# Performance work log

Hardware: AMD Instinct MI355X
Metric: run time of the kernel (lower is better)

## Reference

```python
import jax, jax.numpy as jnp
import numpy as np

N_NODES = 100000

def _scatter_mean(vals, idx, num_segments):
    # vals: [E, D], idx: [E] -> [num_segments, D], mean with zero-degree -> 0 (PyG clamps count to 1)
    s = jax.ops.segment_sum(vals, idx, num_segments=num_segments)
    cnt = jax.ops.segment_sum(jnp.ones((vals.shape[0],), vals.dtype), idx, num_segments=num_segments)
    return s / jnp.maximum(cnt, 1.0)[:, None]

def _conv(x, edge_index, W1, W2, Wr, br):
    src, dst = edge_index[0], edge_index[1]
    n = x.shape[0]
    # flow source_to_target: aggregate lin1(x)[src] at dst
    out1 = _scatter_mean((x @ W1)[src], dst, n)
    # flow target_to_source: aggregate lin2(x)[dst] at src
    out2 = _scatter_mean((x @ W2)[dst], src, n)
    return x @ Wr + br + out1 + out2

def setup_inputs() -> dict:
    key = jax.random.key(0)
    ks = jax.random.split(key, 10)
    d_in, d_h, E = 64, 64, 1250000
    x = jax.random.normal(ks[0], (N_NODES, d_in), dtype=jnp.float32)
    edge_index = jax.random.randint(ks[1], (2, E), 0, N_NODES)
    def lin(k, fan_in, fan_out):
        bound = 1.0 / np.sqrt(fan_in)
        return jax.random.uniform(k, (fan_in, fan_out), jnp.float32, -bound, bound)
    inp = {"x": x, "edge_index": edge_index}
    inp["W1_0"] = lin(ks[2], d_in, d_h)
    inp["W2_0"] = lin(ks[3], d_in, d_h)
    inp["Wr_0"] = lin(ks[4], d_in, d_h)
    inp["br_0"] = jax.random.uniform(ks[5], (d_h,), jnp.float32, -1/np.sqrt(d_in), 1/np.sqrt(d_in))
    inp["W1_1"] = lin(ks[6], d_h, d_h)
    inp["W2_1"] = lin(ks[7], d_h, d_h)
    inp["Wr_1"] = lin(ks[8], d_h, d_h)
    inp["br_1"] = jax.random.uniform(ks[9], (d_h,), jnp.float32, -1/np.sqrt(d_h), 1/np.sqrt(d_h))
    return inp

def reference(x, edge_index, W1_0, W2_0, Wr_0, br_0, W1_1, W2_1, Wr_1, br_1):
    h = jax.nn.relu(_conv(x, edge_index, W1_0, W2_0, Wr_0, br_0))
    h = jax.nn.relu(_conv(h, edge_index, W1_1, W2_1, Wr_1, br_1))
    return h
```

## Files before the change

kernel.cpp:

```cpp
#include <hip/hip_runtime.h>


typedef __bf16 bf16x8 __attribute__((ext_vector_type(8)));
typedef float  f32x4  __attribute__((ext_vector_type(4)));

#define BSHIFT 9
#define NBMAX  256
#define CAPLOG 13
#define CAP    (1 << CAPLOG)

__launch_bounds__(256)
__global__ void k_bin(const int* __restrict__ ei, int E,
                      int* __restrict__ gcnt ,
                      unsigned* __restrict__ binbuf ) {
    __shared__ int lcnt[2 * NBMAX];
    const int tid = threadIdx.x;
    lcnt[tid] = 0; lcnt[NBMAX + tid] = 0;
    __syncthreads();
    const int start = blockIdx.x * 8192;
    const int end = min(start + 8192, E);
    for (int e = start + tid; e < end; e += 256) {
        int s = ei[e], d = ei[E + e];
        atomicAdd(&lcnt[d >> BSHIFT], 1);
        atomicAdd(&lcnt[NBMAX + (s >> BSHIFT)], 1);
    }
    __syncthreads();
    {
        int c0 = lcnt[tid], c1 = lcnt[NBMAX + tid];
        int b0 = c0 ? atomicAdd(&gcnt[tid], c0) : 0;
        int b1 = c1 ? atomicAdd(&gcnt[NBMAX + tid], c1) : 0;
        lcnt[tid] = b0; lcnt[NBMAX + tid] = b1;
    }
    __syncthreads();
    for (int e = start + tid; e < end; e += 256) {
        int s = ei[e], d = ei[E + e];
        int bi = d >> BSHIFT;
        int p = atomicAdd(&lcnt[bi], 1);
        if (p < CAP)
            binbuf[(bi << CAPLOG) + p] = ((unsigned)(d & 511) << 17) | (unsigned)s;
        int bo = s >> BSHIFT;
        int p2 = atomicAdd(&lcnt[NBMAX + bo], 1);
        if (p2 < CAP)
            binbuf[((NBMAX + bo) << CAPLOG) + p2] = ((unsigned)(s & 511) << 17) | (unsigned)d;
    }
}

__launch_bounds__(256)
__global__ void k_scanbase(const int* __restrict__ gcnt, int* __restrict__ gbase) {
    __shared__ int sm[NBMAX];
    const int tid = threadIdx.x;
    int v = gcnt[blockIdx.x * NBMAX + tid];
    sm[tid] = v;
    __syncthreads();
    for (int off = 1; off < NBMAX; off <<= 1) {
        int t = (tid >= off) ? sm[tid - off] : 0;
        __syncthreads();
        sm[tid] += t;
        __syncthreads();
    }
    gbase[blockIdx.x * NBMAX + tid] = sm[tid] - v;
}

__launch_bounds__(256)
__global__ void k_binfill2(const unsigned* __restrict__ binbuf, const int* __restrict__ gcnt,
                           const int* __restrict__ gbase, int n,
                           int* __restrict__ rp_in, int* __restrict__ rp_out,
                           int* __restrict__ ci_in, int* __restrict__ ci_out) {
    __shared__ int h[512];
    __shared__ int cur[512];
    __shared__ int s_tot;
    const int dir = blockIdx.y, bkt = blockIdx.x, tid = threadIdx.x;
    int* rp = dir ? rp_out : rp_in;
    int* ci = dir ? ci_out : ci_in;
    h[tid] = 0; h[256 + tid] = 0;
    __syncthreads();
    const int cnt = min(gcnt[dir * NBMAX + bkt], CAP);
    const unsigned* buf = binbuf + (((size_t)dir * NBMAX + bkt) << CAPLOG);
    for (int i = tid; i < cnt; i += 256)
        atomicAdd(&h[buf[i] >> 17], 1);
    __syncthreads();
    for (int d = 1; d < 512; d <<= 1) {
        int idx = (tid + 1) * (d << 1) - 1;
        if (idx < 512) h[idx] += h[idx - d];
        __syncthreads();
    }
    if (tid == 0) { s_tot = h[511]; h[511] = 0; }
    __syncthreads();
    for (int d = 256; d >= 1; d >>= 1) {
        int idx = (tid + 1) * (d << 1) - 1;
        if (idx < 512) { int t = h[idx - d]; h[idx - d] = h[idx]; h[idx] += t; }
        __syncthreads();
    }
    const int base_off = gbase[dir * NBMAX + bkt];
    const int nodebase = bkt << BSHIFT;
    for (int i = tid; i < 512; i += 256) {
        int nd = nodebase + i;
        int v = base_off + h[i];
        cur[i] = v;
        if (nd < n) rp[nd] = v;
    }
    if (tid == 0 && ((n - 1) >> BSHIFT) == bkt)
        rp[n] = base_off + s_tot;
    __syncthreads();
    for (int i = tid; i < cnt; i += 256) {
        unsigned ent = buf[i];
        int slot = atomicAdd(&cur[ent >> 17], 1);
        ci[slot] = (int)(ent & 0x1FFFFu);
    }
}

__global__ void k_prep(const float* __restrict__ W1, const float* __restrict__ W2,
                       const float* __restrict__ Wr,
                       __bf16* __restrict__ WcT_h, __bf16* __restrict__ WcT_l,
                       __bf16* __restrict__ WrT_h, __bf16* __restrict__ WrT_l) {
    int i = blockIdx.x * 256 + threadIdx.x;
    if (i < 8192) {
        int nn = i >> 7, k = i & 127;
        float w = (k < 64) ? W1[k * 64 + nn] : W2[(k - 64) * 64 + nn];
        __bf16 h = (__bf16)w;
        WcT_h[i] = h;
        WcT_l[i] = (__bf16)(w - (float)h);
    } else if (i < 12288) {
        int j = i - 8192;
        int nn = j >> 6, k = j & 63;
        float w = Wr[k * 64 + nn];
        __bf16 h = (__bf16)w;
        WrT_h[j] = h;
        WrT_l[j] = (__bf16)(w - (float)h);
    }
}

__launch_bounds__(256, 8)
__global__ void k_gather(const float* __restrict__ Hin,
                         const int* __restrict__ rp_in, const int* __restrict__ ci_in,
                         const int* __restrict__ rp_out, const int* __restrict__ ci_out,
                         __bf16* __restrict__ Ah, __bf16* __restrict__ Al, int n) {
    const int lane = threadIdx.x & 63;
    const int wid  = threadIdx.x >> 6;
    const int v = blockIdx.x * 4 + wid;
    if (v >= n) return;
    const int q = lane & 15, sub = lane >> 4;

    #pragma unroll
    for (int dir = 0; dir < 2; ++dir) {
        const int* rp = dir ? rp_out : rp_in;
        const int* ci = dir ? ci_out : ci_in;
        int s = rp[v], e = rp[v + 1];
        float ax = 0.f, ay = 0.f, az = 0.f, aw = 0.f;
        int t = s;
        for (; t + 8 <= e; t += 8) {
            int u0 = ci[t + sub];
            int u1 = ci[t + 4 + sub];
            float4 f0 = *(const float4*)(Hin + (size_t)u0 * 64 + q * 4);
            float4 f1 = *(const float4*)(Hin + (size_t)u1 * 64 + q * 4);
            ax += f0.x + f1.x; ay += f0.y + f1.y;
            az += f0.z + f1.z; aw += f0.w + f1.w;
        }
        for (; t < e; t += 4) {
            int r = t + sub;
            if (r < e) {
                int u = ci[r];
                float4 f = *(const float4*)(Hin + (size_t)u * 64 + q * 4);
                ax += f.x; ay += f.y; az += f.z; aw += f.w;
            }
        }
        ax += __shfl_xor(ax, 16, 64); ax += __shfl_xor(ax, 32, 64);
        ay += __shfl_xor(ay, 16, 64); ay += __shfl_xor(ay, 32, 64);
        az += __shfl_xor(az, 16, 64); az += __shfl_xor(az, 32, 64);
        aw += __shfl_xor(aw, 16, 64); aw += __shfl_xor(aw, 32, 64);
        float inv = 1.0f / (float)max(e - s, 1);
        ax *= inv; ay *= inv; az *= inv; aw *= inv;

        if (sub == 0) {
            union { __bf16 h[4]; uint2 u2; } ph, pl;
            float m[4] = {ax, ay, az, aw};
            #pragma unroll
            for (int c = 0; c < 4; ++c) {
                __bf16 h = (__bf16)m[c];
                ph.h[c] = h;
                pl.h[c] = (__bf16)(m[c] - (float)h);
            }
            size_t off = (size_t)v * 128 + dir * 64 + q * 4;
            *(uint2*)(Ah + off) = ph.u2;
            *(uint2*)(Al + off) = pl.u2;
        }
    }
}

__global__ void k_gemm(const __bf16* __restrict__ Ah, const __bf16* __restrict__ Al,
                       const float* __restrict__ Hin,
                       const __bf16* __restrict__ WcT_h, const __bf16* __restrict__ WcT_l,
                       const __bf16* __restrict__ WrT_h, const __bf16* __restrict__ WrT_l,
                       const float* __restrict__ br, float* __restrict__ Hout, int n) {
    const int lane = threadIdx.x & 63;
    const int wid  = threadIdx.x >> 6;
    const int q = lane & 15, sub = lane >> 4;
    const int rowbase = blockIdx.x * 64 + wid * 16;
    const int arow = min(rowbase + q, n - 1);

    f32x4 acc[4];
    #pragma unroll
    for (int nf = 0; nf < 4; ++nf) acc[nf] = (f32x4){0.f, 0.f, 0.f, 0.f};

    #pragma unroll
    for (int ks = 0; ks < 4; ++ks) {
        const size_t ao = (size_t)arow * 128 + ks * 32 + sub * 8;
        bf16x8 a_h = *(const bf16x8*)(Ah + ao);
        bf16x8 a_l = *(const bf16x8*)(Al + ao);
        #pragma unroll
        for (int nf = 0; nf < 4; ++nf) {
            const size_t bo = (size_t)(nf * 16 + q) * 128 + ks * 32 + sub * 8;
            bf16x8 b_h = *(const bf16x8*)(WcT_h + bo);
            bf16x8 b_l = *(const bf16x8*)(WcT_l + bo);
            acc[nf] = __builtin_amdgcn_mfma_f32_16x16x32_bf16(a_h, b_h, acc[nf], 0, 0, 0);
            acc[nf] = __builtin_amdgcn_mfma_f32_16x16x32_bf16(a_h, b_l, acc[nf], 0, 0, 0);
            acc[nf] = __builtin_amdgcn_mfma_f32_16x16x32_bf16(a_l, b_h, acc[nf], 0, 0, 0);
        }
    }
    #pragma unroll
    for (int ks = 0; ks < 2; ++ks) {
        const float* hp = Hin + (size_t)arow * 64 + ks * 32 + sub * 8;
        float4 h0 = *(const float4*)hp;
        float4 h1 = *(const float4*)(hp + 4);
        float hf[8] = {h0.x, h0.y, h0.z, h0.w, h1.x, h1.y, h1.z, h1.w};
        bf16x8 a_h, a_l;
        #pragma unroll
        for (int c = 0; c < 8; ++c) {
            __bf16 h = (__bf16)hf[c];
            a_h[c] = h;
            a_l[c] = (__bf16)(hf[c] - (float)h);
        }
        #pragma unroll
        for (int nf = 0; nf < 4; ++nf) {
            const size_t bo = (size_t)(nf * 16 + q) * 64 + ks * 32 + sub * 8;
            bf16x8 b_h = *(const bf16x8*)(WrT_h + bo);
            bf16x8 b_l = *(const bf16x8*)(WrT_l + bo);
            acc[nf] = __builtin_amdgcn_mfma_f32_16x16x32_bf16(a_h, b_h, acc[nf], 0, 0, 0);
            acc[nf] = __builtin_amdgcn_mfma_f32_16x16x32_bf16(a_h, b_l, acc[nf], 0, 0, 0);
            acc[nf] = __builtin_amdgcn_mfma_f32_16x16x32_bf16(a_l, b_h, acc[nf], 0, 0, 0);
        }
    }
    #pragma unroll
    for (int nf = 0; nf < 4; ++nf) {
        int col = nf * 16 + q;
        float b = br[col];
        #pragma unroll
        for (int reg = 0; reg < 4; ++reg) {
            int row = rowbase + sub * 4 + reg;
            if (row < n)
                Hout[(size_t)row * 64 + col] = fmaxf(acc[nf][reg] + b, 0.f);
        }
    }
}

extern "C" void kernel_launch(void* const* d_in, const int* in_sizes, int n_in,
                              void* d_out, int out_size, void* d_ws, size_t ws_size,
                              hipStream_t stream) {
    const float* x    = (const float*)d_in[0];
    const int*   ei   = (const int*)d_in[1];
    const float* W1_0 = (const float*)d_in[2];
    const float* W2_0 = (const float*)d_in[3];
    const float* Wr_0 = (const float*)d_in[4];
    const float* br_0 = (const float*)d_in[5];
    const float* W1_1 = (const float*)d_in[6];
    const float* W2_1 = (const float*)d_in[7];
    const float* Wr_1 = (const float*)d_in[8];
    const float* br_1 = (const float*)d_in[9];
    float* out = (float*)d_out;

    const int N = in_sizes[0] / 64;
    const int E = in_sizes[1] / 2;
    const int NB = (N + 511) >> BSHIFT;

    char* p = (char*)d_ws;
    auto alloc = [&](size_t bytes) { char* r = p; p += (bytes + 255) & ~255ULL; return r; };

    int* rp_in   = (int*)alloc(((size_t)N + 1) * 4);
    int* rp_out  = (int*)alloc(((size_t)N + 1) * 4);
    int* gcnt    = (int*)alloc(2 * NBMAX * 4);
    int* gbase   = (int*)alloc(2 * NBMAX * 4);
    int* ci_in   = (int*)alloc((size_t)E * 4);
    int* ci_out  = (int*)alloc((size_t)E * 4);
    __bf16* Ah   = (__bf16*)alloc((size_t)N * 128 * 2);
    __bf16* Al   = (__bf16*)alloc((size_t)N * 128 * 2);
    float* H     = (float*)alloc((size_t)N * 64 * 4);
    __bf16* WcT_h0 = (__bf16*)alloc(8192 * 2);
    __bf16* WcT_l0 = (__bf16*)alloc(8192 * 2);
    __bf16* WrT_h0 = (__bf16*)alloc(4096 * 2);
    __bf16* WrT_l0 = (__bf16*)alloc(4096 * 2);
    __bf16* WcT_h1 = (__bf16*)alloc(8192 * 2);
    __bf16* WcT_l1 = (__bf16*)alloc(8192 * 2);
    __bf16* WrT_h1 = (__bf16*)alloc(4096 * 2);
    __bf16* WrT_l1 = (__bf16*)alloc(4096 * 2);

    unsigned* binbuf = (unsigned*)Ah;

    hipMemsetAsync(gcnt, 0, 2 * NBMAX * 4, stream);

    int bb = (E + 8191) / 8192;
    k_bin<<<bb, 256, 0, stream>>>(ei, E, gcnt, binbuf);
    k_scanbase<<<2, NBMAX, 0, stream>>>(gcnt, gbase);
    k_binfill2<<<dim3(NB, 2), 256, 0, stream>>>(binbuf, gcnt, gbase, N,
                                                rp_in, rp_out, ci_in, ci_out);

    k_prep<<<48, 256, 0, stream>>>(W1_0, W2_0, Wr_0, WcT_h0, WcT_l0, WrT_h0, WrT_l0);
    k_prep<<<48, 256, 0, stream>>>(W1_1, W2_1, Wr_1, WcT_h1, WcT_l1, WrT_h1, WrT_l1);

    int gb = (N + 3) / 4;
    int mb = (N + 63) / 64;

    k_gather<<<gb, 256, 0, stream>>>(x, rp_in, ci_in, rp_out, ci_out, Ah, Al, N);
    k_gemm<<<mb, 256, 0, stream>>>(Ah, Al, x, WcT_h0, WcT_l0, WrT_h0, WrT_l0, br_0, H, N);

    k_gather<<<gb, 256, 0, stream>>>(H, rp_in, ci_in, rp_out, ci_out, Ah, Al, N);
    k_gemm<<<mb, 256, 0, stream>>>(Ah, Al, H, WcT_h1, WcT_l1, WrT_h1, WrT_l1, br_1, out, N);
}
```

Measured before the change: 427.9 us.

## Fuse bucket scan into binfill, merge weight prep launches, interleave gather directions

Drops the separate bucket-base scan kernel, so each binfill block recomputes the 256-entry prefix scan of bucket counts in shared memory. The two weight-prep launches become one 2D-grid launch. The gather kernel now walks the in- and out-edge lists together in one loop, four neighbours per direction per iteration, and does a single combined shuffle reduction. Launch bounds drop from 8 to 6 waves. This cuts launch count and gives more independent loads in flight per wave, at the cost of redundant scan work and more registers per thread.

```diff
diff --git a/kernel.cpp b/kernel.cpp
--- a/kernel.cpp
+++ b/kernel.cpp
@@ -46,34 +46,27 @@
 }
 
 __launch_bounds__(256)
-__global__ void k_scanbase(const int* __restrict__ gcnt, int* __restrict__ gbase) {
-    __shared__ int sm[NBMAX];
-    const int tid = threadIdx.x;
-    int v = gcnt[blockIdx.x * NBMAX + tid];
-    sm[tid] = v;
-    __syncthreads();
-    for (int off = 1; off < NBMAX; off <<= 1) {
-        int t = (tid >= off) ? sm[tid - off] : 0;
-        __syncthreads();
-        sm[tid] += t;
-        __syncthreads();
-    }
-    gbase[blockIdx.x * NBMAX + tid] = sm[tid] - v;
-}
-
-__launch_bounds__(256)
 __global__ void k_binfill2(const unsigned* __restrict__ binbuf, const int* __restrict__ gcnt,
-                           const int* __restrict__ gbase, int n,
+                           int n,
                            int* __restrict__ rp_in, int* __restrict__ rp_out,
                            int* __restrict__ ci_in, int* __restrict__ ci_out) {
     __shared__ int h[512];
     __shared__ int cur[512];
+    __shared__ int gb[NBMAX];
     __shared__ int s_tot;
     const int dir = blockIdx.y, bkt = blockIdx.x, tid = threadIdx.x;
     int* rp = dir ? rp_out : rp_in;
     int* ci = dir ? ci_out : ci_in;
     h[tid] = 0; h[256 + tid] = 0;
-    __syncthreads();
+    gb[tid] = gcnt[dir * NBMAX + tid];
+    __syncthreads();
+    for (int off = 1; off < NBMAX; off <<= 1) {
+        int t = (tid >= off) ? gb[tid - off] : 0;
+        __syncthreads();
+        gb[tid] += t;
+        __syncthreads();
+    }
+    const int base_off = bkt ? gb[bkt - 1] : 0;
     const int cnt = min(gcnt[dir * NBMAX + bkt], CAP);
     const unsigned* buf = binbuf + (((size_t)dir * NBMAX + bkt) << CAPLOG);
     for (int i = tid; i < cnt; i += 256)
@@ -91,7 +84,6 @@
         if (idx < 512) { int t = h[idx - d]; h[idx - d] = h[idx]; h[idx] += t; }
         __syncthreads();
     }
-    const int base_off = gbase[dir * NBMAX + bkt];
     const int nodebase = bkt << BSHIFT;
     for (int i = tid; i < 512; i += 256) {
         int nd = nodebase + i;
@@ -109,28 +101,36 @@
     }
 }
 
-__global__ void k_prep(const float* __restrict__ W1, const float* __restrict__ W2,
-                       const float* __restrict__ Wr,
-                       __bf16* __restrict__ WcT_h, __bf16* __restrict__ WcT_l,
-                       __bf16* __restrict__ WrT_h, __bf16* __restrict__ WrT_l) {
+__global__ void k_prep2(const float* __restrict__ W1a, const float* __restrict__ W2a,
+                        const float* __restrict__ Wra,
+                        __bf16* __restrict__ WcTha, __bf16* __restrict__ WcTla,
+                        __bf16* __restrict__ WrTha, __bf16* __restrict__ WrTla,
+                        const float* __restrict__ W1b, const float* __restrict__ W2b,
+                        const float* __restrict__ Wrb,
+                        __bf16* __restrict__ WcThb, __bf16* __restrict__ WcTlb,
+                        __bf16* __restrict__ WrThb, __bf16* __restrict__ WrTlb) {
+    const float *W1, *W2, *Wr;
+    __bf16 *Wch, *Wcl, *Wrh, *Wrl;
+    if (blockIdx.y == 0) { W1 = W1a; W2 = W2a; Wr = Wra; Wch = WcTha; Wcl = WcTla; Wrh = WrTha; Wrl = WrTla; }
+    else                 { W1 = W1b; W2 = W2b; Wr = Wrb; Wch = WcThb; Wcl = WcTlb; Wrh = WrThb; Wrl = WrTlb; }
     int i = blockIdx.x * 256 + threadIdx.x;
     if (i < 8192) {
         int nn = i >> 7, k = i & 127;
         float w = (k < 64) ? W1[k * 64 + nn] : W2[(k - 64) * 64 + nn];
         __bf16 h = (__bf16)w;
-        WcT_h[i] = h;
-        WcT_l[i] = (__bf16)(w - (float)h);
+        Wch[i] = h;
+        Wcl[i] = (__bf16)(w - (float)h);
     } else if (i < 12288) {
         int j = i - 8192;
         int nn = j >> 6, k = j & 63;
         float w = Wr[k * 64 + nn];
         __bf16 h = (__bf16)w;
-        WrT_h[j] = h;
-        WrT_l[j] = (__bf16)(w - (float)h);
-    }
-}
-
-__launch_bounds__(256, 8)
+        Wrh[j] = h;
+        Wrl[j] = (__bf16)(w - (float)h);
+    }
+}
+
+__launch_bounds__(256, 6)
 __global__ void k_gather(const float* __restrict__ Hin,
                          const int* __restrict__ rp_in, const int* __restrict__ ci_in,
                          const int* __restrict__ rp_out, const int* __restrict__ ci_out,
@@ -141,39 +141,46 @@
     if (v >= n) return;
     const int q = lane & 15, sub = lane >> 4;
 
-    #pragma unroll
-    for (int dir = 0; dir < 2; ++dir) {
-        const int* rp = dir ? rp_out : rp_in;
-        const int* ci = dir ? ci_out : ci_in;
-        int s = rp[v], e = rp[v + 1];
-        float ax = 0.f, ay = 0.f, az = 0.f, aw = 0.f;
-        int t = s;
-        for (; t + 8 <= e; t += 8) {
-            int u0 = ci[t + sub];
-            int u1 = ci[t + 4 + sub];
-            float4 f0 = *(const float4*)(Hin + (size_t)u0 * 64 + q * 4);
-            float4 f1 = *(const float4*)(Hin + (size_t)u1 * 64 + q * 4);
-            ax += f0.x + f1.x; ay += f0.y + f1.y;
-            az += f0.z + f1.z; aw += f0.w + f1.w;
-        }
-        for (; t < e; t += 4) {
-            int r = t + sub;
-            if (r < e) {
-                int u = ci[r];
-                float4 f = *(const float4*)(Hin + (size_t)u * 64 + q * 4);
-                ax += f.x; ay += f.y; az += f.z; aw += f.w;
+    const int s0 = rp_in[v],  e0 = rp_in[v + 1],  len0 = e0 - s0;
+    const int s1 = rp_out[v], e1 = rp_out[v + 1], len1 = e1 - s1;
+    const int mlen = max(len0, len1);
+    const float* __restrict__ hq = Hin + q * 4;
+
+    float4 a0 = {0.f, 0.f, 0.f, 0.f}, a1 = {0.f, 0.f, 0.f, 0.f};
+    for (int t = sub; t < mlen; t += 16) {
+        #pragma unroll
+        for (int u = 0; u < 4; ++u) {
+            int r = t + u * 4;
+            if (r < len0) {
+                int nd = ci_in[s0 + r];
+                float4 f = *(const float4*)(hq + (size_t)nd * 64);
+                a0.x += f.x; a0.y += f.y; a0.z += f.z; a0.w += f.w;
             }
-        }
-        ax += __shfl_xor(ax, 16, 64); ax += __shfl_xor(ax, 32, 64);
-        ay += __shfl_xor(ay, 16, 64); ay += __shfl_xor(ay, 32, 64);
-        az += __shfl_xor(az, 16, 64); az += __shfl_xor(az, 32, 64);
-        aw += __shfl_xor(aw, 16, 64); aw += __shfl_xor(aw, 32, 64);
-        float inv = 1.0f / (float)max(e - s, 1);
-        ax *= inv; ay *= inv; az *= inv; aw *= inv;
-
-        if (sub == 0) {
+            if (r < len1) {
+                int nd = ci_out[s1 + r];
+                float4 f = *(const float4*)(hq + (size_t)nd * 64);
+                a1.x += f.x; a1.y += f.y; a1.z += f.z; a1.w += f.w;
+            }
+        }
+    }
+    #pragma unroll
+    for (int m = 16; m <= 32; m <<= 1) {
+        a0.x += __shfl_xor(a0.x, m, 64); a0.y += __shfl_xor(a0.y, m, 64);
+        a0.z += __shfl_xor(a0.z, m, 64); a0.w += __shfl_xor(a0.w, m, 64);
+        a1.x += __shfl_xor(a1.x, m, 64); a1.y += __shfl_xor(a1.y, m, 64);
+        a1.z += __shfl_xor(a1.z, m, 64); a1.w += __shfl_xor(a1.w, m, 64);
+    }
+    float inv0 = 1.0f / (float)max(len0, 1);
+    float inv1 = 1.0f / (float)max(len1, 1);
+    a0.x *= inv0; a0.y *= inv0; a0.z *= inv0; a0.w *= inv0;
+    a1.x *= inv1; a1.y *= inv1; a1.z *= inv1; a1.w *= inv1;
+
+    if (sub == 0) {
+        #pragma unroll
+        for (int dir = 0; dir < 2; ++dir) {
+            float m[4] = {dir ? a1.x : a0.x, dir ? a1.y : a0.y,
+                          dir ? a1.z : a0.z, dir ? a1.w : a0.w};
             union { __bf16 h[4]; uint2 u2; } ph, pl;
-            float m[4] = {ax, ay, az, aw};
             #pragma unroll
             for (int c = 0; c < 4; ++c) {
                 __bf16 h = (__bf16)m[c];
@@ -278,7 +285,6 @@
     int* rp_in   = (int*)alloc(((size_t)N + 1) * 4);
     int* rp_out  = (int*)alloc(((size_t)N + 1) * 4);
     int* gcnt    = (int*)alloc(2 * NBMAX * 4);
-    int* gbase   = (int*)alloc(2 * NBMAX * 4);
     int* ci_in   = (int*)alloc((size_t)E * 4);
     int* ci_out  = (int*)alloc((size_t)E * 4);
     __bf16* Ah   = (__bf16*)alloc((size_t)N * 128 * 2);
@@ -299,12 +305,10 @@
 
     int bb = (E + 8191) / 8192;
     k_bin<<<bb, 256, 0, stream>>>(ei, E, gcnt, binbuf);
-    k_scanbase<<<2, NBMAX, 0, stream>>>(gcnt, gbase);
-    k_binfill2<<<dim3(NB, 2), 256, 0, stream>>>(binbuf, gcnt, gbase, N,
+    k_binfill2<<<dim3(NB, 2), 256, 0, stream>>>(binbuf, gcnt, N,
                                                 rp_in, rp_out, ci_in, ci_out);
-
-    k_prep<<<48, 256, 0, stream>>>(W1_0, W2_0, Wr_0, WcT_h0, WcT_l0, WrT_h0, WrT_l0);
-    k_prep<<<48, 256, 0, stream>>>(W1_1, W2_1, Wr_1, WcT_h1, WcT_l1, WrT_h1, WrT_l1);
+    k_prep2<<<dim3(48, 2), 256, 0, stream>>>(W1_0, W2_0, Wr_0, WcT_h0, WcT_l0, WrT_h0, WrT_l0,
+                                             W1_1, W2_1, Wr_1, WcT_h1, WcT_l1, WrT_h1, WrT_l1);
 
     int gb = (N + 3) / 4;
     int mb = (N + 63) / 64;
```

Result: slower. 442.3 us (+3.4%).
